# Kernel optimization log

Measured on AMD Instinct MI355X. Metric: run time of the kernel, lower is better.

Reference implementation:

```python
import jax, jax.numpy as jnp
import numpy as np

TOP_K = 5
MIN_DIST = 10
SALIENCY_THR = 0.1
BLUR_K = 5
BLUR_SIGMA = 1.0
BORDER = 12
Q = 0.9
CAND_MULT = 16  # candidate pool = TOP_K * CAND_MULT before min-dist suppression


def _hann(n):
    # torch.hann_window(n, periodic=False)
    return 0.5 * (1.0 - jnp.cos(2.0 * jnp.pi * jnp.arange(n, dtype=jnp.float32) / (n - 1)))


def _gauss_kernel2d():
    r = BLUR_K // 2
    x = jnp.arange(-r, r + 1, dtype=jnp.float32)
    g = jnp.exp(-(x ** 2) / (2.0 * BLUR_SIGMA ** 2))
    g = g / g.sum()
    k2 = g[:, None] * g[None, :]
    return k2[None, None]  # [1,1,k,k]


def _phase_saliency(img):
    """Phase-spectrum saliency: window -> FFT -> phase-only -> iFFT -> |.|^2 -> blur -> minmax norm -> border mask."""
    B, C, H, W = img.shape
    win = (_hann(H)[:, None] * _hann(W)[None, :])[None, None]  # [1,1,H,W]
    x = img * win
    f = jnp.fft.fft2(x)
    recon = jnp.fft.ifft2(jnp.exp(1j * jnp.angle(f)))
    sal = jnp.abs(recon) ** 2
    pad = BLUR_K // 2
    sal = jax.lax.conv_general_dilated(
        sal, _gauss_kernel2d(), (1, 1), [(pad, pad), (pad, pad)],
        dimension_numbers=("NCHW", "OIHW", "NCHW"))
    mn = sal.min(axis=(2, 3), keepdims=True)
    mx = sal.max(axis=(2, 3), keepdims=True)
    sal = (sal - mn) / (mx - mn + 1e-8)
    border = jnp.zeros((H, W), jnp.float32).at[BORDER:H - BORDER, BORDER:W - BORDER].set(1.0)
    return sal * border


def _dynamic_threshold(sal):
    # thr = value of the k-th largest pixel, k = (1-q)*N  (matches torch.topk(flat,k)[..., -1])
    B = sal.shape[0]
    flat = sal.reshape(B, -1)
    n = flat.shape[1]
    k = max(1, int((1.0 - Q) * n))
    vals = jax.lax.top_k(flat, k)[0]
    return vals[:, -1]  # [B]


def _select_points(sal2d, thr):
    """Greedy min-dist (NMS-style) selection of up to TOP_K peaks above thr. Returns (coords[K,2] xy, labels[K])."""
    H, W = sal2d.shape
    M = TOP_K * CAND_MULT
    scores = jnp.where(sal2d >= thr, sal2d, -jnp.inf).reshape(-1)
    vals, idx = jax.lax.top_k(scores, M)
    ys = (idx // W).astype(jnp.float32)
    xs = (idx % W).astype(jnp.float32)
    pts = jnp.stack([xs, ys], axis=-1)  # (x, y) ordering as in original
    valid = jnp.isfinite(vals)

    def body(i, state):
        keep, cnt = state
        d2 = jnp.sum((pts - pts[i]) ** 2, axis=-1)
        near_kept = jnp.any((d2 < float(MIN_DIST ** 2)) & keep)
        ok = valid[i] & (~near_kept) & (cnt < TOP_K)
        return keep.at[i].set(ok), cnt + ok.astype(jnp.int32)

    keep, _ = jax.lax.fori_loop(0, M, body, (jnp.zeros((M,), bool), jnp.int32(0)))
    order = jnp.argsort(jnp.where(keep, 0, 1).astype(jnp.int32))  # stable: kept (in score order) first
    sel = order[:TOP_K]
    kept = keep[sel]
    coords = jnp.where(kept[:, None], pts[sel], -1.0)
    labels = jnp.where(kept, 1, -1).astype(jnp.int32)
    return coords, labels


def setup_inputs() -> dict:
    key = jax.random.key(0)
    img = jax.random.uniform(key, (16, 1, 512, 512), dtype=jnp.float32)
    return {"img": img}


def reference(img):
    sal = _phase_saliency(img)                      # [B,1,H,W]
    thr = jnp.maximum(_dynamic_threshold(sal), SALIENCY_THR)  # dynamic_thr_mode='max'
    coords, labels = jax.vmap(_select_points)(sal[:, 0], thr)
    return coords, labels, sal
```

## Files before the change

kernel.cpp:

```cpp
#include <hip/hip_runtime.h>
#include <math.h>

#define BATCH 16
#define HW 262144
#define KSEL 26214
#define MCAND 80
#define TOPK 5
#define CAP 2048
#define ZEROWORDS 204816


#define GW0 0.05448868454964294f
#define GW1 0.24420134200323332f
#define GW2 0.40261994689424746f

#define FILL_TW512(nthr)                                       \
    for (int i_ = threadIdx.x; i_ < 256; i_ += (nthr)) {       \
        float rev_ = -(float)i_ * (1.0f / 512.0f);             \
        float s_ = __builtin_amdgcn_sinf(rev_);                \
        float c_ = __builtin_amdgcn_cosf(rev_);                \
        tws[i_] = s_;        twc[i_] = c_;                     \
        tws[i_ + 256] = -s_; twc[i_ + 256] = -c_;              \
    }

#define RP(a) ((a) + ((a) >> 4))
#define RSZ 544

#define R4_FWD(rr, ri, q, s4)                                                 \
    {                                                                          \
        const int log2n = 9 - 2 * (s4);                                        \
        const int log2m = log2n - 2;                                           \
        const int m = 1 << log2m;                                              \
        int r = (q) & (m - 1);                                                 \
        int j0 = (((q) >> log2m) << log2n) + r;                                \
        float a0x = rr[RP(j0)],       a0y = ri[RP(j0)];                        \
        float a1x = rr[RP(j0 + m)],   a1y = ri[RP(j0 + m)];                    \
        float a2x = rr[RP(j0 + 2*m)], a2y = ri[RP(j0 + 2*m)];                  \
        float a3x = rr[RP(j0 + 3*m)], a3y = ri[RP(j0 + 3*m)];                  \
        float s02x = a0x + a2x, s02y = a0y + a2y;                              \
        float d02x = a0x - a2x, d02y = a0y - a2y;                              \
        float s13x = a1x + a3x, s13y = a1y + a3y;                              \
        float d13x = a1x - a3x, d13y = a1y - a3y;                              \
        float y0x = s02x + s13x, y0y = s02y + s13y;                            \
        float y2x = s02x - s13x, y2y = s02y - s13y;                            \
        float y1x = d02x + d13y, y1y = d02y - d13x;                            \
        float y3x = d02x - d13y, y3y = d02y + d13x;                            \
        int e = r << (2 * (s4));                                               \
        float c1 = twc[e],   s1 = tws[e];                                      \
        float c2 = twc[2*e], s2 = tws[2*e];                                    \
        float c3 = twc[3*e], s3 = tws[3*e];                                    \
        rr[RP(j0)]       = y0x;             ri[RP(j0)]       = y0y;            \
        rr[RP(j0 + m)]   = y1x*c1 - y1y*s1; ri[RP(j0 + m)]   = y1x*s1 + y1y*c1;\
        rr[RP(j0 + 2*m)] = y2x*c2 - y2y*s2; ri[RP(j0 + 2*m)] = y2x*s2 + y2y*c2;\
        rr[RP(j0 + 3*m)] = y3x*c3 - y3y*s3; ri[RP(j0 + 3*m)] = y3x*s3 + y3y*c3;\
    }

#define R4_INV(rr, ri, q, s4)                                                 \
    {                                                                          \
        const int log2n = 9 - 2 * (s4);                                        \
        const int log2m = log2n - 2;                                           \
        const int m = 1 << log2m;                                              \
        int r = (q) & (m - 1);                                                 \
        int j0 = (((q) >> log2m) << log2n) + r;                                \
        float a0x = rr[RP(j0)],       a0y = ri[RP(j0)];                        \
        float a1x = rr[RP(j0 + m)],   a1y = ri[RP(j0 + m)];                    \
        float a2x = rr[RP(j0 + 2*m)], a2y = ri[RP(j0 + 2*m)];                  \
        float a3x = rr[RP(j0 + 3*m)], a3y = ri[RP(j0 + 3*m)];                  \
        int e = r << (2 * (s4));                                               \
        float c1 = twc[e],   s1 = tws[e];                                      \
        float c2 = twc[2*e], s2 = tws[2*e];                                    \
        float c3 = twc[3*e], s3 = tws[3*e];                                    \
        float t1x = a1x*c1 + a1y*s1,  t1y = a1y*c1 - a1x*s1;                   \
        float t2x = a2x*c2 + a2y*s2,  t2y = a2y*c2 - a2x*s2;                   \
        float t3x = a3x*c3 + a3y*s3,  t3y = a3y*c3 - a3x*s3;                   \
        float s02x = a0x + t2x, s02y = a0y + t2y;                              \
        float d02x = a0x - t2x, d02y = a0y - t2y;                              \
        float s13x = t1x + t3x, s13y = t1y + t3y;                              \
        float d13x = t1x - t3x, d13y = t1y - t3y;                              \
        rr[RP(j0)]       = s02x + s13x;  ri[RP(j0)]       = s02y + s13y;       \
        rr[RP(j0 + 2*m)] = s02x - s13x;  ri[RP(j0 + 2*m)] = s02y - s13y;       \
        rr[RP(j0 + m)]   = d02x - d13y;  ri[RP(j0 + m)]   = d02y + d13x;       \
        rr[RP(j0 + 3*m)] = d02x + d13y;  ri[RP(j0 + 3*m)] = d02y - d13x;       \
    }

#define R4F_REG(x0,y0,x1,y1,x2,y2,x3,y3, e)                                   \
    { float s02x=(x0)+(x2), s02y=(y0)+(y2), d02x=(x0)-(x2), d02y=(y0)-(y2);    \
      float s13x=(x1)+(x3), s13y=(y1)+(y3), d13x=(x1)-(x3), d13y=(y1)-(y3);    \
      float z0x=s02x+s13x, z0y=s02y+s13y;                                      \
      float z2x=s02x-s13x, z2y=s02y-s13y;                                      \
      float z1x=d02x+d13y, z1y=d02y-d13x;                                      \
      float z3x=d02x-d13y, z3y=d02y+d13x;                                      \
      float c1=twc[(e)], s1=tws[(e)], c2=twc[2*(e)], s2=tws[2*(e)];            \
      float c3=twc[3*(e)], s3=tws[3*(e)];                                      \
      x0=z0x; y0=z0y;                                                          \
      x1=z1x*c1-z1y*s1; y1=z1x*s1+z1y*c1;                                      \
      x2=z2x*c2-z2y*s2; y2=z2x*s2+z2y*c2;                                      \
      x3=z3x*c3-z3y*s3; y3=z3x*s3+z3y*c3; }

#define R4I_REG(x0,y0,x1,y1,x2,y2,x3,y3, e)                                   \
    { float c1=twc[(e)], s1=tws[(e)], c2=twc[2*(e)], s2=tws[2*(e)];            \
      float c3=twc[3*(e)], s3=tws[3*(e)];                                      \
      float t1x=(x1)*c1+(y1)*s1, t1y=(y1)*c1-(x1)*s1;                          \
      float t2x=(x2)*c2+(y2)*s2, t2y=(y2)*c2-(x2)*s2;                          \
      float t3x=(x3)*c3+(y3)*s3, t3y=(y3)*c3-(x3)*s3;                          \
      float s02x=(x0)+t2x, s02y=(y0)+t2y, d02x=(x0)-t2x, d02y=(y0)-t2y;        \
      float s13x=t1x+t3x, s13y=t1y+t3y, d13x=t1x-t3x, d13y=t1y-t3y;            \
      x0=s02x+s13x; y0=s02y+s13y;                                              \
      x2=s02x-s13x; y2=s02y-s13y;                                              \
      x1=d02x-d13y; y1=d02y+d13x;                                              \
      x3=d02x+d13y; y3=d02y-d13x; }

__global__ void k_win_rowfft(const float* __restrict__ img, float2* __restrict__ A) {
    __shared__ float re[2 * RSZ], im[2 * RSZ];
    __shared__ float twc[512], tws[512];
    int t = threadIdx.x;
    FILL_TW512(256)
    int lr = t >> 7;
    int u  = t & 127;
    int row = blockIdx.x * 2 + lr;
    int h = row & 511;
    float wr = 0.5f * (1.0f - __builtin_amdgcn_cosf((float)h * (1.0f / 511.0f)));
    const float* p = img + (size_t)row * 512;
    float* rr = re + lr * RSZ;
    float* ri = im + lr * RSZ;
    {
        int i0 = u * 4;
        float4 v = *reinterpret_cast<const float4*>(p + i0);
        float w0 = 0.5f * (1.0f - __builtin_amdgcn_cosf((float)(i0 + 0) * (1.0f / 511.0f)));
        float w1 = 0.5f * (1.0f - __builtin_amdgcn_cosf((float)(i0 + 1) * (1.0f / 511.0f)));
        float w2 = 0.5f * (1.0f - __builtin_amdgcn_cosf((float)(i0 + 2) * (1.0f / 511.0f)));
        float w3 = 0.5f * (1.0f - __builtin_amdgcn_cosf((float)(i0 + 3) * (1.0f / 511.0f)));
        rr[RP(i0 + 0)] = v.x * wr * w0;  ri[RP(i0 + 0)] = 0.0f;
        rr[RP(i0 + 1)] = v.y * wr * w1;  ri[RP(i0 + 1)] = 0.0f;
        rr[RP(i0 + 2)] = v.z * wr * w2;  ri[RP(i0 + 2)] = 0.0f;
        rr[RP(i0 + 3)] = v.w * wr * w3;  ri[RP(i0 + 3)] = 0.0f;
    }
    __syncthreads();
    R4_FWD(rr, ri, u, 0)  __syncthreads();
    R4_FWD(rr, ri, u, 1)  __syncthreads();
    R4_FWD(rr, ri, u, 2)  __syncthreads();
    R4_FWD(rr, ri, u, 3)  __syncthreads();
    #pragma unroll
    for (int kk = 0; kk < 2; ++kk) {
        int j = (kk * 128 + u) << 1;
        float ax = rr[RP(j)], ay = ri[RP(j)], bx = rr[RP(j + 1)], by = ri[RP(j + 1)];
        rr[RP(j)]     = ax + bx;  ri[RP(j)]     = ay + by;
        rr[RP(j + 1)] = ax - bx;  ri[RP(j + 1)] = ay - by;
    }
    __syncthreads();
    float2* out = A + (size_t)row * 512;
    #pragma unroll
    for (int k2 = 0; k2 < 2; ++k2) {
        int i = u * 4 + k2 * 2;
        float4 v = make_float4(rr[RP(i)], ri[RP(i)], rr[RP(i + 1)], ri[RP(i + 1)]);
        *reinterpret_cast<float4*>(&out[i]) = v;
    }
}

#define CSTR 514
__global__ __launch_bounds__(512) void k_colfft(float2* __restrict__ X) {
    __shared__ float re[16 * CSTR];
    __shared__ float im[16 * CSTR];
    __shared__ float twc[512], tws[512];
    int b = blockIdx.x >> 5;
    int c0 = (blockIdx.x & 31) * 16;
    int t = threadIdx.x;
    FILL_TW512(512)
    float2* base = X + (size_t)b * HW + c0;
    #pragma unroll
    for (int ii = 0; ii < 8; ++ii) {
        int linear = ii * 512 + t;
        int cp = linear & 7;
        int e  = linear >> 3;
        const float4 v = *reinterpret_cast<const float4*>(&base[(size_t)e * 512 + cp * 2]);
        int a0 = (cp * 2) * CSTR + e;
        int a1 = a0 + CSTR;
        re[a0] = v.x; im[a0] = v.y;
        re[a1] = v.z; im[a1] = v.w;
    }
    __syncthreads();
    int c = t & 15, tt = t >> 4;
    float* cr = re + c * CSTR;
    float* ci = im + c * CSTR;
    float rx[4][4], ry[4][4];

    #pragma unroll
    for (int a = 0; a < 4; ++a)
        #pragma unroll
        for (int bq = 0; bq < 4; ++bq) {
            int j = tt + a * 128 + bq * 32;
            rx[a][bq] = cr[j]; ry[a][bq] = ci[j];
        }
    #pragma unroll
    for (int bq = 0; bq < 4; ++bq) {
        int e = tt + bq * 32;
        R4F_REG(rx[0][bq], ry[0][bq], rx[1][bq], ry[1][bq],
                rx[2][bq], ry[2][bq], rx[3][bq], ry[3][bq], e)
    }
    {
        int e = tt << 2;
        #pragma unroll
        for (int a = 0; a < 4; ++a)
            R4F_REG(rx[a][0], ry[a][0], rx[a][1], ry[a][1],
                    rx[a][2], ry[a][2], rx[a][3], ry[a][3], e)
    }
    #pragma unroll
    for (int a = 0; a < 4; ++a)
        #pragma unroll
        for (int bq = 0; bq < 4; ++bq) {
            int j = tt + a * 128 + bq * 32;
            cr[j] = rx[a][bq]; ci[j] = ry[a][bq];
        }
    __syncthreads();

    {
        int blk = tt >> 1, r = tt & 1;
        int jb = blk * 32 + r;
        #pragma unroll
        for (int a = 0; a < 4; ++a)
            #pragma unroll
            for (int bq = 0; bq < 4; ++bq) {
                int j = jb + a * 8 + bq * 2;
                rx[a][bq] = cr[j]; ry[a][bq] = ci[j];
            }
        #pragma unroll
        for (int bq = 0; bq < 4; ++bq) {
            int e = (r + 2 * bq) << 4;
            R4F_REG(rx[0][bq], ry[0][bq], rx[1][bq], ry[1][bq],
                    rx[2][bq], ry[2][bq], rx[3][bq], ry[3][bq], e)
        }
        {
            int e = r << 6;
            #pragma unroll
            for (int a = 0; a < 4; ++a)
                R4F_REG(rx[a][0], ry[a][0], rx[a][1], ry[a][1],
                        rx[a][2], ry[a][2], rx[a][3], ry[a][3], e)
        }
        #pragma unroll
        for (int a = 0; a < 4; ++a)
            #pragma unroll
            for (int bq = 0; bq < 4; ++bq) {
                int j = jb + a * 8 + bq * 2;
                cr[j] = rx[a][bq]; ci[j] = ry[a][bq];
            }
    }
    __syncthreads();
    #pragma unroll
    for (int kk = 0; kk < 8; ++kk) {
        int j = (kk * 32 + tt) << 1;
        float ax = cr[j], ay = ci[j], bx = cr[j+1], by = ci[j+1];
        cr[j]   = ax + bx; ci[j]   = ay + by;
        cr[j+1] = ax - bx; ci[j+1] = ay - by;
    }
    __syncthreads();
    #pragma unroll
    for (int ii = 0; ii < 16; ++ii) {
        int linear = ii * 512 + t;
        int cc = linear & 15, e = linear >> 4;
        int a = cc * CSTR + e;
        float x = re[a], y = im[a];
        float m2 = x * x + y * y;
        if (m2 > 0.0f) {
            float inv = rsqrtf(m2);
            re[a] = x * inv; im[a] = y * inv;
        } else {
            re[a] = 1.0f; im[a] = 0.0f;
        }
    }
    __syncthreads();
    #pragma unroll
    for (int kk = 0; kk < 8; ++kk) {
        int j = (kk * 32 + tt) << 1;
        float ax = cr[j], ay = ci[j], bx = cr[j+1], by = ci[j+1];
        cr[j]   = ax + bx; ci[j]   = ay + by;
        cr[j+1] = ax - bx; ci[j+1] = ay - by;
    }
    __syncthreads();
    {
        int blk = tt >> 1, r = tt & 1;
        int jb = blk * 32 + r;
        #pragma unroll
        for (int a = 0; a < 4; ++a)
            #pragma unroll
            for (int bq = 0; bq < 4; ++bq) {
                int j = jb + a * 8 + bq * 2;
                rx[a][bq] = cr[j]; ry[a][bq] = ci[j];
            }
        {
            int e = r << 6;
            #pragma unroll
            for (int a = 0; a < 4; ++a)
                R4I_REG(rx[a][0], ry[a][0], rx[a][1], ry[a][1],
                        rx[a][2], ry[a][2], rx[a][3], ry[a][3], e)
        }
        #pragma unroll
        for (int bq = 0; bq < 4; ++bq) {
            int e = (r + 2 * bq) << 4;
            R4I_REG(rx[0][bq], ry[0][bq], rx[1][bq], ry[1][bq],
                    rx[2][bq], ry[2][bq], rx[3][bq], ry[3][bq], e)
        }
        #pragma unroll
        for (int a = 0; a < 4; ++a)
            #pragma unroll
            for (int bq = 0; bq < 4; ++bq) {
                int j = jb + a * 8 + bq * 2;
                cr[j] = rx[a][bq]; ci[j] = ry[a][bq];
            }
    }
    __syncthreads();
    #pragma unroll
    for (int a = 0; a < 4; ++a)
        #pragma unroll
        for (int bq = 0; bq < 4; ++bq) {
            int j = tt + a * 128 + bq * 32;
            rx[a][bq] = cr[j]; ry[a][bq] = ci[j];
        }
    {
        int e = tt << 2;
        #pragma unroll
        for (int a = 0; a < 4; ++a)
            R4I_REG(rx[a][0], ry[a][0], rx[a][1], ry[a][1],
                    rx[a][2], ry[a][2], rx[a][3], ry[a][3], e)
    }
    #pragma unroll
    for (int bq = 0; bq < 4; ++bq) {
        int e = tt + bq * 32;
        R4I_REG(rx[0][bq], ry[0][bq], rx[1][bq], ry[1][bq],
                rx[2][bq], ry[2][bq], rx[3][bq], ry[3][bq], e)
    }
    #pragma unroll
    for (int a = 0; a < 4; ++a)
        #pragma unroll
        for (int bq = 0; bq < 4; ++bq) {
            int j = tt + a * 128 + bq * 32;
            cr[j] = rx[a][bq]; ci[j] = ry[a][bq];
        }
    __syncthreads();
    #pragma unroll
    for (int ii = 0; ii < 8; ++ii) {
        int linear = ii * 512 + t;
        int cp = linear & 7;
        int e  = linear >> 3;
        int a0 = (cp * 2) * CSTR + e;
        int a1 = a0 + CSTR;
        float4 v = make_float4(re[a0], im[a0], re[a1], im[a1]);
        *reinterpret_cast<float4*>(&base[(size_t)e * 512 + cp * 2]) = v;
    }
}

__global__ void k_mag_hblur(const float2* __restrict__ X, float* __restrict__ out) {
    __shared__ float re[2 * RSZ], im[2 * RSZ];
    __shared__ float twc[512], tws[512];
    int t = threadIdx.x;
    FILL_TW512(256)
    int lr = t >> 7;
    int u  = t & 127;
    int row = blockIdx.x * 2 + lr;
    const float2* p = X + (size_t)row * 512;
    float* rr = re + lr * RSZ;
    float* ri = im + lr * RSZ;
    #pragma unroll
    for (int k2 = 0; k2 < 2; ++k2) {
        int i = u * 4 + k2 * 2;
        float4 v = *reinterpret_cast<const float4*>(&p[i]);
        rr[RP(i)]     = v.x; ri[RP(i)]     = v.y;
        rr[RP(i + 1)] = v.z; ri[RP(i + 1)] = v.w;
    }
    __syncthreads();
    #pragma unroll
    for (int kk = 0; kk < 2; ++kk) {
        int j = (kk * 128 + u) << 1;
        float ax = rr[RP(j)], ay = ri[RP(j)], bx = rr[RP(j + 1)], by = ri[RP(j + 1)];
        rr[RP(j)]     = ax + bx;  ri[RP(j)]     = ay + by;
        rr[RP(j + 1)] = ax - bx;  ri[RP(j + 1)] = ay - by;
    }
    __syncthreads();
    R4_INV(rr, ri, u, 3)  __syncthreads();
    R4_INV(rr, ri, u, 2)  __syncthreads();
    R4_INV(rr, ri, u, 1)  __syncthreads();
    R4_INV(rr, ri, u, 0)  __syncthreads();
    const float s = 3.814697265625e-06f;
    #pragma unroll
    for (int k4 = 0; k4 < 4; ++k4) {
        int i = u * 4 + k4;
        float x = rr[RP(i)] * s, y = ri[RP(i)] * s;
        ri[RP(i)] = x * x + y * y;
    }
    __syncthreads();
    float* o = out + (size_t)row * 512;
    float4 res;
    #pragma unroll
    for (int k4 = 0; k4 < 4; ++k4) {
        int i = u * 4 + k4;
        float acc = GW2 * ri[RP(i)];
        if (i >= 1)   acc += GW1 * ri[RP(i - 1)];
        if (i >= 2)   acc += GW0 * ri[RP(i - 2)];
        if (i <= 510) acc += GW1 * ri[RP(i + 1)];
        if (i <= 509) acc += GW0 * ri[RP(i + 2)];
        ((float*)&res)[k4] = acc;
    }
    *reinterpret_cast<float4*>(o + u * 4) = res;
}

__global__ void k_vblur(const float* __restrict__ in, float* __restrict__ out,
                        float* __restrict__ pmn, float* __restrict__ pmx,
                        unsigned int* __restrict__ zr) {
    __shared__ float smn[256];
    __shared__ float smx[256];
    int t = threadIdx.x;
    int gi = blockIdx.x * 256 + t;
    if (gi < ZEROWORDS) zr[gi] = 0u;
    int i = gi * 4;
    int y = (i >> 9) & 511;
    const float4 c = *reinterpret_cast<const float4*>(in + i);
    float4 acc = make_float4(GW2 * c.x, GW2 * c.y, GW2 * c.z, GW2 * c.w);
    if (y >= 1) {
        const float4 v = *reinterpret_cast<const float4*>(in + i - 512);
        acc.x += GW1 * v.x; acc.y += GW1 * v.y; acc.z += GW1 * v.z; acc.w += GW1 * v.w;
    }
    if (y >= 2) {
        const float4 v = *reinterpret_cast<const float4*>(in + i - 1024);
        acc.x += GW0 * v.x; acc.y += GW0 * v.y; acc.z += GW0 * v.z; acc.w += GW0 * v.w;
    }
    if (y <= 510) {
        const float4 v = *reinterpret_cast<const float4*>(in + i + 512);
        acc.x += GW1 * v.x; acc.y += GW1 * v.y; acc.z += GW1 * v.z; acc.w += GW1 * v.w;
    }
    if (y <= 509) {
        const float4 v = *reinterpret_cast<const float4*>(in + i + 1024);
        acc.x += GW0 * v.x; acc.y += GW0 * v.y; acc.z += GW0 * v.z; acc.w += GW0 * v.w;
    }
    *reinterpret_cast<float4*>(out + i) = acc;
    float lmn = fminf(fminf(acc.x, acc.y), fminf(acc.z, acc.w));
    float lmx = fmaxf(fmaxf(acc.x, acc.y), fmaxf(acc.z, acc.w));
    smn[t] = lmn; smx[t] = lmx;
    __syncthreads();
    for (int s = 128; s > 0; s >>= 1) {
        if (t < s) { smn[t] = fminf(smn[t], smn[t + s]); smx[t] = fmaxf(smx[t], smx[t + s]); }
        __syncthreads();
    }
    if (t == 0) { pmn[blockIdx.x] = smn[0]; pmx[blockIdx.x] = smx[0]; }
}

__global__ void k_norm_hist(const float* __restrict__ in, const float* __restrict__ pmn,
                            const float* __restrict__ pmx, float* __restrict__ out,
                            unsigned int* __restrict__ g) {
    __shared__ unsigned int h[4096];
    __shared__ float smn[256], smx[256];
    int t = threadIdx.x;
    int b = blockIdx.x >> 5;
    int base = b * HW + (blockIdx.x & 31) * 8192;
    smn[t] = pmn[b * 256 + t];
    smx[t] = pmx[b * 256 + t];
    for (int i = t; i < 4096; i += 256) h[i] = 0u;
    __syncthreads();
    for (int s = 128; s > 0; s >>= 1) {
        if (t < s) { smn[t] = fminf(smn[t], smn[t + s]); smx[t] = fmaxf(smx[t], smx[t + s]); }
        __syncthreads();
    }
    float mn = smn[0], mx = smx[0];
    float inv = 1.0f / (mx - mn + 1e-8f);
    for (int j = 0; j < 32; ++j) {
        int idx = base + j * 256 + t;
        float v = (in[idx] - mn) * inv;
        int xx = idx & 511, yy = (idx >> 9) & 511;
        bool inside = (xx >= 12) && (xx < 500) && (yy >= 12) && (yy < 500);
        v = inside ? v : 0.0f;
        out[idx] = v;
        atomicAdd(&h[__float_as_uint(v) >> 20], 1u);
    }
    __syncthreads();
    unsigned int* gb = g + b * 4096;
    for (int i = t; i < 4096; i += 256)
        if (h[i]) atomicAdd(&gb[i], h[i]);
}

__device__ void radix_step(const unsigned int* __restrict__ h, int nbins, int krem,
                           int t, unsigned int* tsuf, int* sbin, int* skrem) {
    int bpt = nbins >> 8;
    unsigned int s = 0;
    for (int j = 0; j < bpt; ++j) s += h[t * bpt + j];
    tsuf[t] = s;
    __syncthreads();
    #pragma unroll
    for (int off = 1; off < 256; off <<= 1) {
        unsigned int v = (t + off < 256) ? tsuf[t + off] : 0u;
        __syncthreads();
        tsuf[t] += v;
        __syncthreads();
    }
    if ((int)tsuf[t] >= krem && (t == 255 || (int)tsuf[t + 1] < krem))
        *sbin = t;
    __syncthreads();
    int seg = *sbin;
    int krem2 = krem - (seg < 255 ? (int)tsuf[seg + 1] : 0);
    __syncthreads();
    if (t < bpt) {
        unsigned int L = 0;
        for (int j = t; j < bpt; ++j) L += h[seg * bpt + j];
        unsigned int hv = h[seg * bpt + t];
        if ((int)L >= krem2 && (int)(L - hv) < krem2) {
            *sbin  = seg * bpt + t;
            *skrem = krem2 - (int)(L - hv);
        }
    }
    __syncthreads();
}

__global__ void k_hist2(const float* __restrict__ sal, const unsigned int* __restrict__ g1,
                        unsigned int* __restrict__ gA, unsigned int* __restrict__ gB,
                        unsigned int* prefA1, int* kremA1, unsigned int* prefB1, int* kremB1) {
    __shared__ unsigned int hA[4096];
    __shared__ unsigned int hB[4096];
    __shared__ unsigned int tsuf[256];
    __shared__ int sbin, skrem;
    int t = threadIdx.x;
    int b = blockIdx.x >> 5;
    int start = (blockIdx.x & 31) * 8192;
    for (int i = t; i < 4096; i += 256) { hA[i] = 0u; hB[i] = 0u; }
    radix_step(g1 + b * 4096, 4096, KSEL, t, tsuf, &sbin, &skrem);
    unsigned int pA = (unsigned int)sbin; int krA = skrem;
    radix_step(g1 + b * 4096, 4096, MCAND, t, tsuf, &sbin, &skrem);
    unsigned int pB = (unsigned int)sbin; int krB = skrem;
    if (t == 0 && (blockIdx.x & 31) == 0) {
        prefA1[b] = pA; kremA1[b] = krA; prefB1[b] = pB; kremB1[b] = krB;
    }
    const float* p = sal + (size_t)b * HW;
    for (int j = 0; j < 32; ++j) {
        unsigned int u = __float_as_uint(p[start + j * 256 + t]);
        unsigned int hi = u >> 20, mid = (u >> 8) & 4095u;
        if (hi == pA) atomicAdd(&hA[mid], 1u);
        if (hi == pB) atomicAdd(&hB[mid], 1u);
    }
    __syncthreads();
    unsigned int* ga = gA + b * 4096;
    unsigned int* gb2 = gB + b * 4096;
    for (int i = t; i < 4096; i += 256) {
        if (hA[i]) atomicAdd(&ga[i], hA[i]);
        if (hB[i]) atomicAdd(&gb2[i], hB[i]);
    }
}

__global__ void k_hist3collect(const float* __restrict__ sal,
                               const unsigned int* __restrict__ gA2, const unsigned int* __restrict__ gB2,
                               const unsigned int* prefA1, const int* kremA1,
                               const unsigned int* prefB1, const int* kremB1,
                               unsigned int* __restrict__ gA3,
                               unsigned int* prefA24, int* kremA2,
                               float* __restrict__ candv, int* __restrict__ candi,
                               int* __restrict__ ccnt) {
    __shared__ unsigned int hA[256];
    __shared__ unsigned int tsuf[256];
    __shared__ int sbin, skrem;
    int t = threadIdx.x;
    int b = blockIdx.x >> 5;
    int start = (blockIdx.x & 31) * 8192;
    hA[t] = 0u;
    radix_step(gA2 + b * 4096, 4096, kremA1[b], t, tsuf, &sbin, &skrem);
    unsigned int pA = (prefA1[b] << 12) | (unsigned int)sbin;
    int krA2 = skrem;
    radix_step(gB2 + b * 4096, 4096, kremB1[b], t, tsuf, &sbin, &skrem);
    unsigned int cutB = ((prefB1[b] << 12) | (unsigned int)sbin) << 8;
    if (t == 0 && (blockIdx.x & 31) == 0) { prefA24[b] = pA; kremA2[b] = krA2; }
    const float* p = sal + (size_t)b * HW;
    for (int j = 0; j < 32; ++j) {
        int i = start + j * 256 + t;
        unsigned int u = __float_as_uint(p[i]);
        if ((u >> 8) == pA) atomicAdd(&hA[u & 255u], 1u);
        if (u >= cutB) {
            int pos = atomicAdd(&ccnt[b], 1);
            if (pos < CAP) { candv[b * CAP + pos] = p[i]; candi[b * CAP + pos] = i; }
        }
    }
    __syncthreads();
    if (hA[t]) atomicAdd(&gA3[b * 256 + t], hA[t]);
}

__global__ void k_final(const unsigned int* __restrict__ gA3,
                        const unsigned int* prefA24, const int* kremA2,
                        const float* __restrict__ candv, const int* __restrict__ candi,
                        const int* __restrict__ ccnt, float* __restrict__ out) {
    __shared__ float cval[CAP];
    __shared__ int   cidx[CAP];
    __shared__ int   si[MCAND];
    __shared__ float svv[MCAND];
    __shared__ float sx[MCAND];
    __shared__ float sy[MCAND];
    __shared__ unsigned long long nearLo[MCAND];
    __shared__ unsigned long long nearHi[MCAND];
    __shared__ unsigned int tsuf[256];
    __shared__ int sbin, skrem;
    int b = blockIdx.x, t = threadIdx.x;
    radix_step(gA3 + b * 256, 256, kremA2[b], t, tsuf, &sbin, &skrem);
    float thr = fmaxf(__uint_as_float((prefA24[b] << 8) | (unsigned int)sbin), 0.1f);
    int n = min(ccnt[b], CAP);
    for (int i = t; i < n; i += 256) { cval[i] = candv[b * CAP + i]; cidx[i] = candi[b * CAP + i]; }
    __syncthreads();
    int m = min(n, MCAND);
    for (int i = t; i < n; i += 256) {
        float vi = cval[i]; int ii = cidx[i];
        int rank = 0;
        for (int j = 0; j < n; j++) {
            float vj = cval[j];
            if (vj > vi || (vj == vi && cidx[j] < ii)) rank++;
        }
        if (rank < MCAND) { si[rank] = ii; svv[rank] = vi; }
    }
    __syncthreads();
    for (int i = t; i < m; i += 256) {
        sx[i] = (float)(si[i] & 511);
        sy[i] = (float)(si[i] >> 9);
    }
    __syncthreads();
    for (int i = t; i < m; i += 256) {
        unsigned long long lo = 0ull, hi = 0ull;
        float x = sx[i], y = sy[i];
        for (int j = 0; j < m; j++) {
            float dx = sx[j] - x, dy = sy[j] - y;
            if (dx * dx + dy * dy < 100.0f) {
                if (j < 64) lo |= (1ull << j);
                else        hi |= (1ull << (j - 64));
            }
        }
        nearLo[i] = lo; nearHi[i] = hi;
    }
    __syncthreads();
    if (t == 0) {
        unsigned long long kLo = 0ull, kHi = 0ull;
        int cnt = 0;
        for (int i = 0; i < m; i++) {
            bool near_kept = ((nearLo[i] & kLo) | (nearHi[i] & kHi)) != 0ull;
            if (svv[i] >= thr && !near_kept) {
                out[b * 10 + 2 * cnt]     = sx[i];
                out[b * 10 + 2 * cnt + 1] = sy[i];
                out[160 + b * 5 + cnt]    = 1.0f;
                if (i < 64) kLo |= (1ull << i); else kHi |= (1ull << (i - 64));
                cnt++;
                if (cnt == TOPK) break;
            }
        }
        for (int j = cnt; j < TOPK; j++) {
            out[b * 10 + 2 * j]     = -1.0f;
            out[b * 10 + 2 * j + 1] = -1.0f;
            out[160 + b * 5 + j]    = -1.0f;
        }
    }
}

extern "C" void kernel_launch(void* const* d_in, const int* in_sizes, int n_in,
                              void* d_out, int out_size, void* d_ws, size_t ws_size,
                              hipStream_t stream) {
    const float* img = (const float*)d_in[0];
    float* out = (float*)d_out;
    char* ws = (char*)d_ws;

    float2* A    = (float2*)ws;
    float*  hb   = (float*)(ws + 33554432UL);
    float*  salb = (float*)(ws + 50331648UL);

    unsigned int* hist1  = (unsigned int*)(ws + 0UL);
    unsigned int* hist2a = (unsigned int*)(ws + 262144UL);
    unsigned int* hist2b = (unsigned int*)(ws + 524288UL);
    unsigned int* hist3a = (unsigned int*)(ws + 786432UL);
    int*          ccnt   = (int*)(ws + 819200UL);
    float*        candv  = (float*)(ws + 851968UL);
    int*          candi  = (int*)(ws + 983040UL);

    float* pmn = (float*)(ws + 20971520UL);
    float* pmx = (float*)(ws + 21037056UL);

    char* stats = ws + 67108864UL;
    unsigned int* prefA1  = (unsigned int*)(stats + 0);
    int*          kremA1  = (int*)(stats + 64);
    unsigned int* prefB1  = (unsigned int*)(stats + 128);
    int*          kremB1  = (int*)(stats + 192);
    unsigned int* prefA24 = (unsigned int*)(stats + 256);
    int*          kremA2  = (int*)(stats + 320);

    float* salout = out + 240;

    k_win_rowfft<<<dim3(4096), dim3(256), 0, stream>>>(img, A);
    k_colfft<<<dim3(512), dim3(512), 0, stream>>>(A);
    k_mag_hblur<<<dim3(4096), dim3(256), 0, stream>>>(A, hb);
    k_vblur<<<dim3(4096), dim3(256), 0, stream>>>(hb, salb, pmn, pmx,
                                                  (unsigned int*)ws);
    k_norm_hist<<<dim3(512), dim3(256), 0, stream>>>(salb, pmn, pmx, salout, hist1);
    k_hist2<<<dim3(512), dim3(256), 0, stream>>>(salout, hist1, hist2a, hist2b,
                                                 prefA1, kremA1, prefB1, kremB1);
    k_hist3collect<<<dim3(512), dim3(256), 0, stream>>>(salout, hist2a, hist2b,
                                                        prefA1, kremA1, prefB1, kremB1,
                                                        hist3a, prefA24, kremA2,
                                                        candv, candi, ccnt);
    k_final<<<dim3(BATCH), dim3(256), 0, stream>>>(hist3a, prefA24, kremA2,
                                                   candv, candi, ccnt, out);
}
```

Before: 152.4 us.

## Use register radix-16 passes for row FFTs and fuse phase normalization into radix-2

```diff
diff --git a/kernel.cpp b/kernel.cpp
--- a/kernel.cpp
+++ b/kernel.cpp
@@ -25,63 +25,6 @@
 
 #define RP(a) ((a) + ((a) >> 4))
 #define RSZ 544
-
-#define R4_FWD(rr, ri, q, s4)                                                 \
-    {                                                                          \
-        const int log2n = 9 - 2 * (s4);                                        \
-        const int log2m = log2n - 2;                                           \
-        const int m = 1 << log2m;                                              \
-        int r = (q) & (m - 1);                                                 \
-        int j0 = (((q) >> log2m) << log2n) + r;                                \
-        float a0x = rr[RP(j0)],       a0y = ri[RP(j0)];                        \
-        float a1x = rr[RP(j0 + m)],   a1y = ri[RP(j0 + m)];                    \
-        float a2x = rr[RP(j0 + 2*m)], a2y = ri[RP(j0 + 2*m)];                  \
-        float a3x = rr[RP(j0 + 3*m)], a3y = ri[RP(j0 + 3*m)];                  \
-        float s02x = a0x + a2x, s02y = a0y + a2y;                              \
-        float d02x = a0x - a2x, d02y = a0y - a2y;                              \
-        float s13x = a1x + a3x, s13y = a1y + a3y;                              \
-        float d13x = a1x - a3x, d13y = a1y - a3y;                              \
-        float y0x = s02x + s13x, y0y = s02y + s13y;                            \
-        float y2x = s02x - s13x, y2y = s02y - s13y;                            \
-        float y1x = d02x + d13y, y1y = d02y - d13x;                            \
-        float y3x = d02x - d13y, y3y = d02y + d13x;                            \
-        int e = r << (2 * (s4));                                               \
-        float c1 = twc[e],   s1 = tws[e];                                      \
-        float c2 = twc[2*e], s2 = tws[2*e];                                    \
-        float c3 = twc[3*e], s3 = tws[3*e];                                    \
-        rr[RP(j0)]       = y0x;             ri[RP(j0)]       = y0y;            \
-        rr[RP(j0 + m)]   = y1x*c1 - y1y*s1; ri[RP(j0 + m)]   = y1x*s1 + y1y*c1;\
-        rr[RP(j0 + 2*m)] = y2x*c2 - y2y*s2; ri[RP(j0 + 2*m)] = y2x*s2 + y2y*c2;\
-        rr[RP(j0 + 3*m)] = y3x*c3 - y3y*s3; ri[RP(j0 + 3*m)] = y3x*s3 + y3y*c3;\
-    }
-
-#define R4_INV(rr, ri, q, s4)                                                 \
-    {                                                                          \
-        const int log2n = 9 - 2 * (s4);                                        \
-        const int log2m = log2n - 2;                                           \
-        const int m = 1 << log2m;                                              \
-        int r = (q) & (m - 1);                                                 \
-        int j0 = (((q) >> log2m) << log2n) + r;                                \
-        float a0x = rr[RP(j0)],       a0y = ri[RP(j0)];                        \
-        float a1x = rr[RP(j0 + m)],   a1y = ri[RP(j0 + m)];                    \
-        float a2x = rr[RP(j0 + 2*m)], a2y = ri[RP(j0 + 2*m)];                  \
-        float a3x = rr[RP(j0 + 3*m)], a3y = ri[RP(j0 + 3*m)];                  \
-        int e = r << (2 * (s4));                                               \
-        float c1 = twc[e],   s1 = tws[e];                                      \
-        float c2 = twc[2*e], s2 = tws[2*e];                                    \
-        float c3 = twc[3*e], s3 = tws[3*e];                                    \
-        float t1x = a1x*c1 + a1y*s1,  t1y = a1y*c1 - a1x*s1;                   \
-        float t2x = a2x*c2 + a2y*s2,  t2y = a2y*c2 - a2x*s2;                   \
-        float t3x = a3x*c3 + a3y*s3,  t3y = a3y*c3 - a3x*s3;                   \
-        float s02x = a0x + t2x, s02y = a0y + t2y;                              \
-        float d02x = a0x - t2x, d02y = a0y - t2y;                              \
-        float s13x = t1x + t3x, s13y = t1y + t3y;                              \
-        float d13x = t1x - t3x, d13y = t1y - t3y;                              \
-        rr[RP(j0)]       = s02x + s13x;  ri[RP(j0)]       = s02y + s13y;       \
-        rr[RP(j0 + 2*m)] = s02x - s13x;  ri[RP(j0 + 2*m)] = s02y - s13y;       \
-        rr[RP(j0 + m)]   = d02x - d13y;  ri[RP(j0 + m)]   = d02y + d13x;       \
-        rr[RP(j0 + 3*m)] = d02x + d13y;  ri[RP(j0 + 3*m)] = d02y - d13x;       \
-    }
 
 #define R4F_REG(x0,y0,x1,y1,x2,y2,x3,y3, e)                                   \
     { float s02x=(x0)+(x2), s02y=(y0)+(y2), d02x=(x0)-(x2), d02y=(y0)-(y2);    \
@@ -110,50 +53,106 @@
       x1=d02x-d13y; y1=d02y+d13x;                                              \
       x3=d02x+d13y; y3=d02y-d13x; }
 
+#define LD_P1(rr, ri)                                                          \
+    _Pragma("unroll") for (int a = 0; a < 4; ++a)                              \
+    _Pragma("unroll") for (int bq = 0; bq < 4; ++bq) {                         \
+        int j = tt + a * 128 + bq * 32;                                        \
+        rx[a][bq] = rr[RP(j)]; ry[a][bq] = ri[RP(j)]; }
+#define ST_P1(rr, ri)                                                          \
+    _Pragma("unroll") for (int a = 0; a < 4; ++a)                              \
+    _Pragma("unroll") for (int bq = 0; bq < 4; ++bq) {                         \
+        int j = tt + a * 128 + bq * 32;                                        \
+        rr[RP(j)] = rx[a][bq]; ri[RP(j)] = ry[a][bq]; }
+#define LD_P2(rr, ri)                                                          \
+    _Pragma("unroll") for (int a = 0; a < 4; ++a)                              \
+    _Pragma("unroll") for (int bq = 0; bq < 4; ++bq) {                         \
+        int j = jb + a * 8 + bq * 2;                                           \
+        rx[a][bq] = rr[RP(j)]; ry[a][bq] = ri[RP(j)]; }
+#define ST_P2(rr, ri)                                                          \
+    _Pragma("unroll") for (int a = 0; a < 4; ++a)                              \
+    _Pragma("unroll") for (int bq = 0; bq < 4; ++bq) {                         \
+        int j = jb + a * 8 + bq * 2;                                           \
+        rr[RP(j)] = rx[a][bq]; ri[RP(j)] = ry[a][bq]; }
+
+#define PAIR1_FWD                                                              \
+    _Pragma("unroll") for (int bq = 0; bq < 4; ++bq) {                         \
+        int e = tt + bq * 32;                                                  \
+        R4F_REG(rx[0][bq], ry[0][bq], rx[1][bq], ry[1][bq],                    \
+                rx[2][bq], ry[2][bq], rx[3][bq], ry[3][bq], e) }               \
+    { int e = tt << 2;                                                         \
+      _Pragma("unroll") for (int a = 0; a < 4; ++a)                            \
+          R4F_REG(rx[a][0], ry[a][0], rx[a][1], ry[a][1],                      \
+                  rx[a][2], ry[a][2], rx[a][3], ry[a][3], e) }
+#define PAIR2_FWD                                                              \
+    _Pragma("unroll") for (int bq = 0; bq < 4; ++bq) {                         \
+        int e = (r2 + 2 * bq) << 4;                                            \
+        R4F_REG(rx[0][bq], ry[0][bq], rx[1][bq], ry[1][bq],                    \
+                rx[2][bq], ry[2][bq], rx[3][bq], ry[3][bq], e) }               \
+    { int e = r2 << 6;                                                         \
+      _Pragma("unroll") for (int a = 0; a < 4; ++a)                            \
+          R4F_REG(rx[a][0], ry[a][0], rx[a][1], ry[a][1],                      \
+                  rx[a][2], ry[a][2], rx[a][3], ry[a][3], e) }
+#define PAIR2_INV                                                              \
+    { int e = r2 << 6;                                                         \
+      _Pragma("unroll") for (int a = 0; a < 4; ++a)                            \
+          R4I_REG(rx[a][0], ry[a][0], rx[a][1], ry[a][1],                      \
+                  rx[a][2], ry[a][2], rx[a][3], ry[a][3], e) }                 \
+    _Pragma("unroll") for (int bq = 0; bq < 4; ++bq) {                         \
+        int e = (r2 + 2 * bq) << 4;                                            \
+        R4I_REG(rx[0][bq], ry[0][bq], rx[1][bq], ry[1][bq],                    \
+                rx[2][bq], ry[2][bq], rx[3][bq], ry[3][bq], e) }
+#define PAIR1_INV                                                              \
+    { int e = tt << 2;                                                         \
+      _Pragma("unroll") for (int a = 0; a < 4; ++a)                            \
+          R4I_REG(rx[a][0], ry[a][0], rx[a][1], ry[a][1],                      \
+                  rx[a][2], ry[a][2], rx[a][3], ry[a][3], e) }                 \
+    _Pragma("unroll") for (int bq = 0; bq < 4; ++bq) {                         \
+        int e = tt + bq * 32;                                                  \
+        R4I_REG(rx[0][bq], ry[0][bq], rx[1][bq], ry[1][bq],                    \
+                rx[2][bq], ry[2][bq], rx[3][bq], ry[3][bq], e) }
+
 __global__ void k_win_rowfft(const float* __restrict__ img, float2* __restrict__ A) {
-    __shared__ float re[2 * RSZ], im[2 * RSZ];
+    __shared__ float re[8 * RSZ], im[8 * RSZ];
     __shared__ float twc[512], tws[512];
     int t = threadIdx.x;
     FILL_TW512(256)
-    int lr = t >> 7;
-    int u  = t & 127;
-    int row = blockIdx.x * 2 + lr;
+    int lr = t >> 5;
+    int tt = t & 31;
+    int row = blockIdx.x * 8 + lr;
     int h = row & 511;
     float wr = 0.5f * (1.0f - __builtin_amdgcn_cosf((float)h * (1.0f / 511.0f)));
     const float* p = img + (size_t)row * 512;
     float* rr = re + lr * RSZ;
     float* ri = im + lr * RSZ;
-    {
-        int i0 = u * 4;
+    #pragma unroll
+    for (int k = 0; k < 4; ++k) {
+        int i0 = k * 128 + tt * 4;
         float4 v = *reinterpret_cast<const float4*>(p + i0);
-        float w0 = 0.5f * (1.0f - __builtin_amdgcn_cosf((float)(i0 + 0) * (1.0f / 511.0f)));
-        float w1 = 0.5f * (1.0f - __builtin_amdgcn_cosf((float)(i0 + 1) * (1.0f / 511.0f)));
-        float w2 = 0.5f * (1.0f - __builtin_amdgcn_cosf((float)(i0 + 2) * (1.0f / 511.0f)));
-        float w3 = 0.5f * (1.0f - __builtin_amdgcn_cosf((float)(i0 + 3) * (1.0f / 511.0f)));
-        rr[RP(i0 + 0)] = v.x * wr * w0;  ri[RP(i0 + 0)] = 0.0f;
-        rr[RP(i0 + 1)] = v.y * wr * w1;  ri[RP(i0 + 1)] = 0.0f;
-        rr[RP(i0 + 2)] = v.z * wr * w2;  ri[RP(i0 + 2)] = 0.0f;
-        rr[RP(i0 + 3)] = v.w * wr * w3;  ri[RP(i0 + 3)] = 0.0f;
-    }
-    __syncthreads();
-    R4_FWD(rr, ri, u, 0)  __syncthreads();
-    R4_FWD(rr, ri, u, 1)  __syncthreads();
-    R4_FWD(rr, ri, u, 2)  __syncthreads();
-    R4_FWD(rr, ri, u, 3)  __syncthreads();
-    #pragma unroll
-    for (int kk = 0; kk < 2; ++kk) {
-        int j = (kk * 128 + u) << 1;
+        #pragma unroll
+        for (int j = 0; j < 4; ++j) {
+            float wc = 0.5f * (1.0f - __builtin_amdgcn_cosf((float)(i0 + j) * (1.0f / 511.0f)));
+            rr[RP(i0 + j)] = ((const float*)&v)[j] * wr * wc;
+            ri[RP(i0 + j)] = 0.0f;
+        }
+    }
+    __syncthreads();
+    float rx[4][4], ry[4][4];
+    LD_P1(rr, ri)
+    PAIR1_FWD
+    ST_P1(rr, ri)
+    __syncthreads();
+    int r2 = tt & 1, jb = (tt >> 1) * 32 + r2;
+    LD_P2(rr, ri)
+    PAIR2_FWD
+    ST_P2(rr, ri)
+    __syncthreads();
+    float2* out = A + (size_t)row * 512;
+    #pragma unroll
+    for (int kk = 0; kk < 8; ++kk) {
+        int j = (kk * 32 + tt) << 1;
         float ax = rr[RP(j)], ay = ri[RP(j)], bx = rr[RP(j + 1)], by = ri[RP(j + 1)];
-        rr[RP(j)]     = ax + bx;  ri[RP(j)]     = ay + by;
-        rr[RP(j + 1)] = ax - bx;  ri[RP(j + 1)] = ay - by;
-    }
-    __syncthreads();
-    float2* out = A + (size_t)row * 512;
-    #pragma unroll
-    for (int k2 = 0; k2 < 2; ++k2) {
-        int i = u * 4 + k2 * 2;
-        float4 v = make_float4(rr[RP(i)], ri[RP(i)], rr[RP(i + 1)], ri[RP(i + 1)]);
-        *reinterpret_cast<float4*>(&out[i]) = v;
+        float4 v = make_float4(ax + bx, ay + by, ax - bx, ay - by);
+        *reinterpret_cast<float4*>(&out[j]) = v;
     }
 }
 
@@ -191,19 +190,7 @@
             int j = tt + a * 128 + bq * 32;
             rx[a][bq] = cr[j]; ry[a][bq] = ci[j];
         }
-    #pragma unroll
-    for (int bq = 0; bq < 4; ++bq) {
-        int e = tt + bq * 32;
-        R4F_REG(rx[0][bq], ry[0][bq], rx[1][bq], ry[1][bq],
-                rx[2][bq], ry[2][bq], rx[3][bq], ry[3][bq], e)
-    }
-    {
-        int e = tt << 2;
-        #pragma unroll
-        for (int a = 0; a < 4; ++a)
-            R4F_REG(rx[a][0], ry[a][0], rx[a][1], ry[a][1],
-                    rx[a][2], ry[a][2], rx[a][3], ry[a][3], e)
-    }
+    PAIR1_FWD
     #pragma unroll
     for (int a = 0; a < 4; ++a)
         #pragma unroll
@@ -212,101 +199,54 @@
             cr[j] = rx[a][bq]; ci[j] = ry[a][bq];
         }
     __syncthreads();
-
-    {
-        int blk = tt >> 1, r = tt & 1;
-        int jb = blk * 32 + r;
-        #pragma unroll
-        for (int a = 0; a < 4; ++a)
-            #pragma unroll
-            for (int bq = 0; bq < 4; ++bq) {
-                int j = jb + a * 8 + bq * 2;
-                rx[a][bq] = cr[j]; ry[a][bq] = ci[j];
-            }
-        #pragma unroll
-        for (int bq = 0; bq < 4; ++bq) {
-            int e = (r + 2 * bq) << 4;
-            R4F_REG(rx[0][bq], ry[0][bq], rx[1][bq], ry[1][bq],
-                    rx[2][bq], ry[2][bq], rx[3][bq], ry[3][bq], e)
-        }
-        {
-            int e = r << 6;
-            #pragma unroll
-            for (int a = 0; a < 4; ++a)
-                R4F_REG(rx[a][0], ry[a][0], rx[a][1], ry[a][1],
-                        rx[a][2], ry[a][2], rx[a][3], ry[a][3], e)
-        }
-        #pragma unroll
-        for (int a = 0; a < 4; ++a)
-            #pragma unroll
-            for (int bq = 0; bq < 4; ++bq) {
-                int j = jb + a * 8 + bq * 2;
-                cr[j] = rx[a][bq]; ci[j] = ry[a][bq];
-            }
-    }
+    int r2 = tt & 1, jb = (tt >> 1) * 32 + r2;
+    #pragma unroll
+    for (int a = 0; a < 4; ++a)
+        #pragma unroll
+        for (int bq = 0; bq < 4; ++bq) {
+            int j = jb + a * 8 + bq * 2;
+            rx[a][bq] = cr[j]; ry[a][bq] = ci[j];
+        }
+    PAIR2_FWD
+    #pragma unroll
+    for (int a = 0; a < 4; ++a)
+        #pragma unroll
+        for (int bq = 0; bq < 4; ++bq) {
+            int j = jb + a * 8 + bq * 2;
+            cr[j] = rx[a][bq]; ci[j] = ry[a][bq];
+        }
     __syncthreads();
     #pragma unroll
     for (int kk = 0; kk < 8; ++kk) {
         int j = (kk * 32 + tt) << 1;
         float ax = cr[j], ay = ci[j], bx = cr[j+1], by = ci[j+1];
-        cr[j]   = ax + bx; ci[j]   = ay + by;
-        cr[j+1] = ax - bx; ci[j+1] = ay - by;
-    }
-    __syncthreads();
-    #pragma unroll
-    for (int ii = 0; ii < 16; ++ii) {
-        int linear = ii * 512 + t;
-        int cc = linear & 15, e = linear >> 4;
-        int a = cc * CSTR + e;
-        float x = re[a], y = im[a];
-        float m2 = x * x + y * y;
-        if (m2 > 0.0f) {
-            float inv = rsqrtf(m2);
-            re[a] = x * inv; im[a] = y * inv;
-        } else {
-            re[a] = 1.0f; im[a] = 0.0f;
-        }
-    }
-    __syncthreads();
-    #pragma unroll
-    for (int kk = 0; kk < 8; ++kk) {
-        int j = (kk * 32 + tt) << 1;
-        float ax = cr[j], ay = ci[j], bx = cr[j+1], by = ci[j+1];
-        cr[j]   = ax + bx; ci[j]   = ay + by;
-        cr[j+1] = ax - bx; ci[j+1] = ay - by;
-    }
-    __syncthreads();
-    {
-        int blk = tt >> 1, r = tt & 1;
-        int jb = blk * 32 + r;
-        #pragma unroll
-        for (int a = 0; a < 4; ++a)
-            #pragma unroll
-            for (int bq = 0; bq < 4; ++bq) {
-                int j = jb + a * 8 + bq * 2;
-                rx[a][bq] = cr[j]; ry[a][bq] = ci[j];
-            }
-        {
-            int e = r << 6;
-            #pragma unroll
-            for (int a = 0; a < 4; ++a)
-                R4I_REG(rx[a][0], ry[a][0], rx[a][1], ry[a][1],
-                        rx[a][2], ry[a][2], rx[a][3], ry[a][3], e)
-        }
-        #pragma unroll
-        for (int bq = 0; bq < 4; ++bq) {
-            int e = (r + 2 * bq) << 4;
-            R4I_REG(rx[0][bq], ry[0][bq], rx[1][bq], ry[1][bq],
-                    rx[2][bq], ry[2][bq], rx[3][bq], ry[3][bq], e)
-        }
-        #pragma unroll
-        for (int a = 0; a < 4; ++a)
-            #pragma unroll
-            for (int bq = 0; bq < 4; ++bq) {
-                int j = jb + a * 8 + bq * 2;
-                cr[j] = rx[a][bq]; ci[j] = ry[a][bq];
-            }
-    }
+        float ux = ax + bx, uy = ay + by;
+        float vx = ax - bx, vy = ay - by;
+        float m2u = ux * ux + uy * uy;
+        if (m2u > 0.0f) { float iv = rsqrtf(m2u); ux *= iv; uy *= iv; }
+        else            { ux = 1.0f; uy = 0.0f; }
+        float m2v = vx * vx + vy * vy;
+        if (m2v > 0.0f) { float iv = rsqrtf(m2v); vx *= iv; vy *= iv; }
+        else            { vx = 1.0f; vy = 0.0f; }
+        cr[j]   = ux + vx; ci[j]   = uy + vy;
+        cr[j+1] = ux - vx; ci[j+1] = uy - vy;
+    }
+    __syncthreads();
+    #pragma unroll
+    for (int a = 0; a < 4; ++a)
+        #pragma unroll
+        for (int bq = 0; bq < 4; ++bq) {
+            int j = jb + a * 8 + bq * 2;
+            rx[a][bq] = cr[j]; ry[a][bq] = ci[j];
+        }
+    PAIR2_INV
+    #pragma unroll
+    for (int a = 0; a < 4; ++a)
+        #pragma unroll
+        for (int bq = 0; bq < 4; ++bq) {
+            int j = jb + a * 8 + bq * 2;
+            cr[j] = rx[a][bq]; ci[j] = ry[a][bq];
+        }
     __syncthreads();
     #pragma unroll
     for (int a = 0; a < 4; ++a)
@@ -315,19 +255,7 @@
             int j = tt + a * 128 + bq * 32;
             rx[a][bq] = cr[j]; ry[a][bq] = ci[j];
         }
-    {
-        int e = tt << 2;
-        #pragma unroll
-        for (int a = 0; a < 4; ++a)
-            R4I_REG(rx[a][0], ry[a][0], rx[a][1], ry[a][1],
-                    rx[a][2], ry[a][2], rx[a][3], ry[a][3], e)
-    }
-    #pragma unroll
-    for (int bq = 0; bq < 4; ++bq) {
-        int e = tt + bq * 32;
-        R4I_REG(rx[0][bq], ry[0][bq], rx[1][bq], ry[1][bq],
-                rx[2][bq], ry[2][bq], rx[3][bq], ry[3][bq], e)
-    }
+    PAIR1_INV
     #pragma unroll
     for (int a = 0; a < 4; ++a)
         #pragma unroll
@@ -349,57 +277,59 @@
 }
 
 __global__ void k_mag_hblur(const float2* __restrict__ X, float* __restrict__ out) {
-    __shared__ float re[2 * RSZ], im[2 * RSZ];
+    __shared__ float re[8 * RSZ], im[8 * RSZ];
     __shared__ float twc[512], tws[512];
     int t = threadIdx.x;
     FILL_TW512(256)
-    int lr = t >> 7;
-    int u  = t & 127;
-    int row = blockIdx.x * 2 + lr;
+    int lr = t >> 5;
+    int tt = t & 31;
+    int row = blockIdx.x * 8 + lr;
     const float2* p = X + (size_t)row * 512;
     float* rr = re + lr * RSZ;
     float* ri = im + lr * RSZ;
     #pragma unroll
-    for (int k2 = 0; k2 < 2; ++k2) {
-        int i = u * 4 + k2 * 2;
-        float4 v = *reinterpret_cast<const float4*>(&p[i]);
-        rr[RP(i)]     = v.x; ri[RP(i)]     = v.y;
-        rr[RP(i + 1)] = v.z; ri[RP(i + 1)] = v.w;
-    }
-    __syncthreads();
-    #pragma unroll
-    for (int kk = 0; kk < 2; ++kk) {
-        int j = (kk * 128 + u) << 1;
-        float ax = rr[RP(j)], ay = ri[RP(j)], bx = rr[RP(j + 1)], by = ri[RP(j + 1)];
-        rr[RP(j)]     = ax + bx;  ri[RP(j)]     = ay + by;
-        rr[RP(j + 1)] = ax - bx;  ri[RP(j + 1)] = ay - by;
-    }
-    __syncthreads();
-    R4_INV(rr, ri, u, 3)  __syncthreads();
-    R4_INV(rr, ri, u, 2)  __syncthreads();
-    R4_INV(rr, ri, u, 1)  __syncthreads();
-    R4_INV(rr, ri, u, 0)  __syncthreads();
+    for (int kk = 0; kk < 8; ++kk) {
+        int j = (kk * 32 + tt) << 1;
+        float4 v = *reinterpret_cast<const float4*>(&p[j]);
+        rr[RP(j)]     = v.x + v.z;  ri[RP(j)]     = v.y + v.w;
+        rr[RP(j + 1)] = v.x - v.z;  ri[RP(j + 1)] = v.y - v.w;
+    }
+    __syncthreads();
+    float rx[4][4], ry[4][4];
+    int r2 = tt & 1, jb = (tt >> 1) * 32 + r2;
+    LD_P2(rr, ri)
+    PAIR2_INV
+    ST_P2(rr, ri)
+    __syncthreads();
+    LD_P1(rr, ri)
+    PAIR1_INV
     const float s = 3.814697265625e-06f;
     #pragma unroll
-    for (int k4 = 0; k4 < 4; ++k4) {
-        int i = u * 4 + k4;
-        float x = rr[RP(i)] * s, y = ri[RP(i)] * s;
-        ri[RP(i)] = x * x + y * y;
-    }
+    for (int a = 0; a < 4; ++a)
+        #pragma unroll
+        for (int bq = 0; bq < 4; ++bq) {
+            int j = tt + a * 128 + bq * 32;
+            float x = rx[a][bq] * s, y = ry[a][bq] * s;
+            ri[RP(j)] = x * x + y * y;
+        }
     __syncthreads();
     float* o = out + (size_t)row * 512;
-    float4 res;
-    #pragma unroll
-    for (int k4 = 0; k4 < 4; ++k4) {
-        int i = u * 4 + k4;
-        float acc = GW2 * ri[RP(i)];
-        if (i >= 1)   acc += GW1 * ri[RP(i - 1)];
-        if (i >= 2)   acc += GW0 * ri[RP(i - 2)];
-        if (i <= 510) acc += GW1 * ri[RP(i + 1)];
-        if (i <= 509) acc += GW0 * ri[RP(i + 2)];
-        ((float*)&res)[k4] = acc;
-    }
-    *reinterpret_cast<float4*>(o + u * 4) = res;
+    #pragma unroll
+    for (int kk = 0; kk < 4; ++kk) {
+        int i0 = (kk * 32 + tt) * 4;
+        float4 res;
+        #pragma unroll
+        for (int j = 0; j < 4; ++j) {
+            int i = i0 + j;
+            float acc = GW2 * ri[RP(i)];
+            if (i >= 1)   acc += GW1 * ri[RP(i - 1)];
+            if (i >= 2)   acc += GW0 * ri[RP(i - 2)];
+            if (i <= 510) acc += GW1 * ri[RP(i + 1)];
+            if (i <= 509) acc += GW0 * ri[RP(i + 2)];
+            ((float*)&res)[j] = acc;
+        }
+        *reinterpret_cast<float4*>(o + i0) = res;
+    }
 }
 
 __global__ void k_vblur(const float* __restrict__ in, float* __restrict__ out,
@@ -679,9 +609,9 @@
 
     float* salout = out + 240;
 
-    k_win_rowfft<<<dim3(4096), dim3(256), 0, stream>>>(img, A);
+    k_win_rowfft<<<dim3(1024), dim3(256), 0, stream>>>(img, A);
     k_colfft<<<dim3(512), dim3(512), 0, stream>>>(A);
-    k_mag_hblur<<<dim3(4096), dim3(256), 0, stream>>>(A, hb);
+    k_mag_hblur<<<dim3(1024), dim3(256), 0, stream>>>(A, hb);
     k_vblur<<<dim3(4096), dim3(256), 0, stream>>>(hb, salb, pmn, pmx,
                                                   (unsigned int*)ws);
     k_norm_hist<<<dim3(512), dim3(256), 0, stream>>>(salb, pmn, pmx, salout, hist1);
```

Result: faster. 129.5 us (-15.0%).
